# Optimization experiments

Hardware: AMD Instinct MI355X
Metric: run time of the kernel (lower is better)

The kernel has to match this reference:

```python
import jax, jax.numpy as jnp
import numpy as np

B, H, E = 32768, 1024, 512
VOCAB = 1600 * 20  # input_dim * 20


def setup_inputs() -> dict:
    key = jax.random.key(0)
    ks = jax.random.split(key, 13)
    sc_e = 1.0 / np.sqrt(E)
    sc_h = 1.0 / np.sqrt(H)
    sc_2h = 1.0 / np.sqrt(2 * H)
    # weights stored as [in, out] (transpose of torch Linear.weight)
    return {
        "s_t_minus_1": jax.random.normal(ks[0], (B, 1, H), jnp.float32),
        "y_t_minus_1": jax.random.randint(ks[1], (B, 1), 0, VOCAB, jnp.int64 if jax.config.jax_enable_x64 else jnp.int32),
        "c_t": jax.random.normal(ks[2], (B, 1, 2 * H), jnp.float32),
        "emb": jax.random.normal(ks[3], (VOCAB, E), jnp.float32),
        "Wz": jax.random.uniform(ks[4], (E, H), jnp.float32, -sc_e, sc_e),
        "Uz": jax.random.uniform(ks[5], (H, H), jnp.float32, -sc_h, sc_h),
        "Cz": jax.random.uniform(ks[6], (2 * H, H), jnp.float32, -sc_2h, sc_2h),
        "Wr": jax.random.uniform(ks[7], (E, H), jnp.float32, -sc_e, sc_e),
        "Ur": jax.random.uniform(ks[8], (H, H), jnp.float32, -sc_h, sc_h),
        "Cr": jax.random.uniform(ks[9], (2 * H, H), jnp.float32, -sc_2h, sc_2h),
        "W": jax.random.uniform(ks[10], (E, H), jnp.float32, -sc_e, sc_e),
        "U": jax.random.uniform(ks[11], (H, H), jnp.float32, -sc_h, sc_h),
        "C": jax.random.uniform(ks[12], (2 * H, H), jnp.float32, -sc_2h, sc_2h),
    }


def reference(s_t_minus_1, y_t_minus_1, c_t, emb, Wz, Uz, Cz, Wr, Ur, Cr, W, U, C):
    # embedding lookup: (B,1) -> (B,1,E)
    y = emb[y_t_minus_1]
    # gates, all contractions over last axis
    z_t = jax.nn.sigmoid(y @ Wz + s_t_minus_1 @ Uz + c_t @ Cz)  # (B,1,H)
    r_t = jax.nn.sigmoid(y @ Wr + s_t_minus_1 @ Ur + c_t @ Cr)  # (B,1,H)
    s_tilde = jnp.tanh(y @ W + (r_t * s_t_minus_1) @ U + c_t @ C)
    s_t = (1.0 - z_t) * s_t_minus_1 + z_t * s_tilde
    return s_t
```

## Files before the change

### kernel.cpp

```cpp
#include <hip/hip_runtime.h>

typedef unsigned short u16;
typedef float  f32x4   __attribute__((ext_vector_type(4)));
typedef float  f32x16  __attribute__((ext_vector_type(16)));
typedef short  bf16x8  __attribute__((ext_vector_type(8)));
typedef u16    u16x8   __attribute__((ext_vector_type(8)));

#define BROWS 32768
#define KTOT  3584
#define NKT   (KTOT / 64)

static __device__ __forceinline__ u16 f2b(float f) {
    unsigned x = __float_as_uint(f);
    x += 0x7fffu + ((x >> 16) & 1u);
    return (u16)(x >> 16);
}
static __device__ __forceinline__ float b2f(u16 u) {
    return __uint_as_float(((unsigned)u) << 16);
}
static __device__ __forceinline__ float sigm(float x) {
    return 1.f / (1.f + __expf(-x));
}
static __device__ __forceinline__ float tanh_s(float x) {
    float ax = fabsf(x);
    float e  = __expf(-2.f * ax);
    float t  = (1.f - e) / (1.f + e);
    return copysignf(t, x);
}
static __device__ __forceinline__ void gld16(const u16* g, u16* l) {
    __builtin_amdgcn_global_load_lds(
        (const __attribute__((address_space(1))) void*)g,
        (__attribute__((address_space(3))) void*)l, 16, 0, 0);
}

__global__ __launch_bounds__(256) void pack_x(
    const float* __restrict__ s, const int* __restrict__ y,
    const float* __restrict__ c, const float* __restrict__ emb,
    u16* __restrict__ X)
{
    long tid = (long)blockIdx.x * 256 + threadIdx.x;
    int  row = (int)(tid / 448);
    int  seg = (int)(tid % 448);
    int  e0  = seg * 8;
    const float* src;
    if (e0 < 512)        src = emb + (long)y[row] * 512 + e0;
    else if (e0 < 1536)  src = s   + (long)row * 1024 + (e0 - 512);
    else                 src = c   + (long)row * 2048 + (e0 - 1536);
    f32x4 a = *(const f32x4*)src;
    f32x4 b = *(const f32x4*)(src + 4);
    u16x8 o;
    o[0]=f2b(a[0]); o[1]=f2b(a[1]); o[2]=f2b(a[2]); o[3]=f2b(a[3]);
    o[4]=f2b(b[0]); o[5]=f2b(b[1]); o[6]=f2b(b[2]); o[7]=f2b(b[3]);
    *(u16x8*)&X[(long)row * KTOT + e0] = o;
}

__global__ __launch_bounds__(256) void wtrans_all(
    const float* __restrict__ Wz, const float* __restrict__ Uz,
    const float* __restrict__ Cz, const float* __restrict__ Wr,
    const float* __restrict__ Ur, const float* __restrict__ Cr,
    const float* __restrict__ W,  const float* __restrict__ U,
    const float* __restrict__ C,
    u16* __restrict__ WzrT, u16* __restrict__ W2T)
{
    __shared__ float t[32][33];
    int z = blockIdx.z;
    const float* src; u16* dst; int kd;
    switch (z) {
        case 0: src = Wz; dst = WzrT + 0;                  kd = 512;  break;
        case 1: src = Uz; dst = WzrT + 512;                kd = 1024; break;
        case 2: src = Cz; dst = WzrT + 1536;               kd = 2048; break;
        case 3: src = Wr; dst = WzrT + 1024 * KTOT;        kd = 512;  break;
        case 4: src = Ur; dst = WzrT + 1024 * KTOT + 512;  kd = 1024; break;
        case 5: src = Cr; dst = WzrT + 1024 * KTOT + 1536; kd = 2048; break;
        case 6: src = W;  dst = W2T + 0;                   kd = 512;  break;
        case 7: src = U;  dst = W2T + 512;                 kd = 1024; break;
        default: src = C; dst = W2T + 1536;                kd = 2048; break;
    }
    int k0 = blockIdx.x * 32;
    if (k0 >= kd) return;
    int n0 = blockIdx.y * 32;
    int tx = threadIdx.x, ty = threadIdx.y;
    #pragma unroll
    for (int r = ty; r < 32; r += 8)
        t[r][tx] = src[(long)(k0 + r) * 1024 + n0 + tx];
    __syncthreads();
    #pragma unroll
    for (int r = ty; r < 32; r += 8)
        dst[(long)(n0 + r) * KTOT + k0 + tx] = f2b(t[tx][r]);
}


#define RDA32(P,mt,ks) a[mt][ks] = *(const bf16x8*)((P) + (mt)*2048 + ((ks)>>1)*512 + (((ks)&1) ? laneX : laneO))
#define RDB32(P,nt,ks) b[nt][ks] = *(const bf16x8*)((P) + (nt)*2048 + ((ks)>>1)*512 + (((ks)&1) ? laneX : laneO))
#define RDA_T(P,mt) RDA32(P,mt,0); RDA32(P,mt,1); RDA32(P,mt,2); RDA32(P,mt,3)
#define RDB_T(P,nt) RDB32(P,nt,0); RDB32(P,nt,1); RDB32(P,nt,2); RDB32(P,nt,3)
#define MM32(mt,nt,ks) acc[mt][nt] = __builtin_amdgcn_mfma_f32_32x32x16_bf16(a[mt][ks], b[nt][ks], acc[mt][nt], 0, 0, 0)
#define MMQ32(m0,m1,nt) \
    MM32(m0,nt,0); MM32(m1,nt,0); MM32(m0,nt,1); MM32(m1,nt,1); \
    MM32(m0,nt,2); MM32(m1,nt,2); MM32(m0,nt,3); MM32(m1,nt,3)

#define PH_MID \
    __builtin_amdgcn_s_barrier(); \
    asm volatile("s_waitcnt lgkmcnt(0)" ::: "memory"); \
    __builtin_amdgcn_sched_barrier(0); \
    __builtin_amdgcn_s_setprio(1);

#define PH_END \
    __builtin_amdgcn_s_setprio(0); \
    __builtin_amdgcn_sched_barrier(0); \
    __builtin_amdgcn_s_barrier();

template<int MODE>
__global__ __launch_bounds__(512, 1) void gemm8(
    const u16* __restrict__ Xc, const u16* __restrict__ rsin,
    const u16* __restrict__ Wt,
    u16* __restrict__ zb, u16* __restrict__ rsb,
    const u16* __restrict__ zread, float* __restrict__ out, int NT)
{
    extern __shared__ u16 smem[];

    int bid = blockIdx.x, nwg = gridDim.x;
    int q   = nwg >> 3;
    int wg  = (bid & 7) * q + (bid >> 3);
    int bm  = wg / NT, bn = wg % NT;
    int R0  = bm * 256;
    int C0  = bn * 256;

    int t = threadIdx.x, w = t >> 6, l = t & 63;
    int wr = w >> 2, wc = w & 3;

    int rl   = l >> 2;
    int ccl  = ((l & 3) * 8) ^ ((l >> 5) * 16) ^ (((w >> 1) & 1) * 8);
    int sr0  = w >> 1, sc = w & 1;
    int colb = sc * 32 + ccl;
    int offAx[2][2], offAr[2][2], offB[2][2];
    #pragma unroll
    for (int h = 0; h < 2; h++)
        #pragma unroll
        for (int i = 0; i < 2; i++) {
            int row = h * 128 + (sr0 + i * 4) * 16 + rl;
            offAx[h][i] = (R0 + row) * KTOT + colb;
            offAr[h][i] = (R0 + row) * 1024 + colb - 512;
            offB [h][i] = (C0 + row) * KTOT + colb;
        }

    auto stageA = [&](int kt) {
        int k0 = kt * 64;
        u16* Ld = smem + (kt & 1) * 32768;
        bool useR = (MODE == 1) && (k0 >= 512) && (k0 < 1536);
        #pragma unroll
        for (int h = 0; h < 2; h++)
            #pragma unroll
            for (int i = 0; i < 2; i++) {
                const u16* g = useR ? (rsin + (offAr[h][i] + k0))
                                    : (Xc   + (offAx[h][i] + k0));
                gld16(g, Ld + h * 8192 + (w + i * 8) * 512);
            }
    };
    auto stageB = [&](int kt) {
        int k0 = kt * 64;
        u16* Ld = smem + (kt & 1) * 32768 + 16384;
        #pragma unroll
        for (int h = 0; h < 2; h++)
            #pragma unroll
            for (int i = 0; i < 2; i++)
                gld16(Wt + (offB[h][i] + k0),
                      Ld + h * 8192 + (w + i * 8) * 512);
    };

    int laneO = ((l >> 4) & 1) * 1024 + (l & 15) * 32
              + ((((l >> 5) * 8) ^ (((l >> 3) & 1) * 16)) ^ (((l >> 4) & 1) * 8));
    int laneX = laneO ^ 16;

    f32x16 acc[4][2];
    #pragma unroll
    for (int mt = 0; mt < 4; mt++)
        #pragma unroll
        for (int nt = 0; nt < 2; nt++)
            acc[mt][nt] = (f32x16)(0.f);

    bf16x8 a[4][4], b[2][4];

    int aoff = wr * 8192;
    int boff = 16384 + wc * 4096;
    const u16* Ae = smem + aoff;
    const u16* Be = smem + boff;
    const u16* Ao = Ae + 32768;
    const u16* Bo = Be + 32768;

    stageA(0); stageB(0);
    stageA(1); stageB(1);
    asm volatile("s_waitcnt vmcnt(8)" ::: "memory");
    __builtin_amdgcn_s_barrier();
    RDA_T(Ae, 0); RDA_T(Ae, 1); RDB_T(Be, 0);

    for (int kt = 0; kt < NKT; ++kt) {
        int bs = kt & 1;
        const u16* Ab = smem + bs * 32768 + aoff;
        const u16* Bb = smem + bs * 32768 + boff;
        const u16* An = smem + (bs ^ 1) * 32768 + aoff;
        const u16* Bn = smem + (bs ^ 1) * 32768 + boff;

        PH_MID; MMQ32(0, 1, 0); RDB_T(Bb, 1); PH_END;
        PH_MID; MMQ32(0, 1, 1); RDA_T(Ab, 2); RDA_T(Ab, 3); PH_END;
        if (kt + 2 < NKT) stageB(kt + 2);
        PH_MID; MMQ32(2, 3, 1); PH_END;
        if (kt + 2 < NKT) {
            stageA(kt + 2);
            asm volatile("s_waitcnt vmcnt(8)" ::: "memory");
        } else {
            asm volatile("s_waitcnt vmcnt(0)" ::: "memory");
        }
        PH_MID; MMQ32(2, 3, 0);
        if (kt + 1 < NKT) { RDA_T(An, 0); RDA_T(An, 1); RDB_T(Bn, 0); }
        PH_END;
    }

    int hi4 = (l >> 5) * 4, lc32 = l & 31;
    long R0w = R0 + wr * 128;
    int  C0w = C0 + wc * 64;
    if (MODE == 0) {
        if (C0 < 1024) {
            #pragma unroll
            for (int mt = 0; mt < 4; mt++)
                #pragma unroll
                for (int nt = 0; nt < 2; nt++) {
                    int col = C0w + nt * 32 + lc32;
                    #pragma unroll
                    for (int qq = 0; qq < 4; qq++)
                        #pragma unroll
                        for (int jj = 0; jj < 4; jj++) {
                            long r = R0w + mt * 32 + qq * 8 + hi4 + jj;
                            zb[r * 1024 + col] = f2b(sigm(acc[mt][nt][qq * 4 + jj]));
                        }
                }
        } else {
            #pragma unroll
            for (int mt = 0; mt < 4; mt++)
                #pragma unroll
                for (int nt = 0; nt < 2; nt++) {
                    int h = C0w + nt * 32 + lc32 - 1024;
                    #pragma unroll
                    for (int qq = 0; qq < 4; qq++)
                        #pragma unroll
                        for (int jj = 0; jj < 4; jj++) {
                            long r = R0w + mt * 32 + qq * 8 + hi4 + jj;
                            float sv = b2f(Xc[r * KTOT + 512 + h]);
                            float rr = sigm(acc[mt][nt][qq * 4 + jj]);
                            rsb[r * 1024 + h] = f2b(rr * sv);
                        }
                }
        }
    } else {
        #pragma unroll
        for (int mt = 0; mt < 4; mt++)
            #pragma unroll
            for (int nt = 0; nt < 2; nt++) {
                int col = C0w + nt * 32 + lc32;
                #pragma unroll
                for (int qq = 0; qq < 4; qq++)
                    #pragma unroll
                    for (int jj = 0; jj < 4; jj++) {
                        long r = R0w + mt * 32 + qq * 8 + hi4 + jj;
                        float st = tanh_s(acc[mt][nt][qq * 4 + jj]);
                        float z  = b2f(zread[r * 1024 + col]);
                        float sv = b2f(Xc[r * KTOT + 512 + col]);
                        out[r * 1024 + col] = fmaf(z, st - sv, sv);
                    }
            }
    }
}

extern "C" void kernel_launch(void* const* d_in, const int* in_sizes, int n_in,
                              void* d_out, int out_size, void* d_ws, size_t ws_size,
                              hipStream_t stream)
{
    const float* s   = (const float*)d_in[0];
    const int*   y   = (const int*)  d_in[1];
    const float* c   = (const float*)d_in[2];
    const float* emb = (const float*)d_in[3];
    const float* Wz  = (const float*)d_in[4];
    const float* Uz  = (const float*)d_in[5];
    const float* Cz  = (const float*)d_in[6];
    const float* Wr  = (const float*)d_in[7];
    const float* Ur  = (const float*)d_in[8];
    const float* Cr  = (const float*)d_in[9];
    const float* W   = (const float*)d_in[10];
    const float* U   = (const float*)d_in[11];
    const float* C   = (const float*)d_in[12];
    float* out = (float*)d_out;

    char* ws = (char*)d_ws;
    u16* Xcat = (u16*)(ws);
    u16* rsb  = (u16*)(ws + 234881024);
    u16* zbuf = (u16*)(ws + 301989888);
    u16* WzrT = (u16*)(ws + 369098752);
    u16* W2T  = (u16*)(ws + 383778816);

    hipFuncSetAttribute((const void*)gemm8<0>,
                        hipFuncAttributeMaxDynamicSharedMemorySize, 131072);
    hipFuncSetAttribute((const void*)gemm8<1>,
                        hipFuncAttributeMaxDynamicSharedMemorySize, 131072);

    pack_x<<<BROWS * 448 / 256, 256, 0, stream>>>(s, y, c, emb, Xcat);

    dim3 tb(32, 8);
    wtrans_all<<<dim3(64, 32, 9), tb, 0, stream>>>(
        Wz, Uz, Cz, Wr, Ur, Cr, W, U, C, WzrT, W2T);

    gemm8<0><<<(BROWS / 256) * (2048 / 256), 512, 131072, stream>>>(
        Xcat, nullptr, WzrT, zbuf, rsb, nullptr, nullptr, 2048 / 256);

    gemm8<1><<<(BROWS / 256) * (1024 / 256), 512, 131072, stream>>>(
        Xcat, rsb, W2T, nullptr, nullptr, zbuf, out, 1024 / 256);
}
```

Measured before the change: 835.1 us.

## Switch GEMM main loop to 32-wide K tiles with 4-stage LDS ring buffer

Result: slower. 858.3 us (+2.8%).

```diff
diff --git a/kernel.cpp b/kernel.cpp
--- a/kernel.cpp
+++ b/kernel.cpp
@@ -8,7 +8,7 @@
 
 #define BROWS 32768
 #define KTOT  3584
-#define NKT   (KTOT / 64)
+#define NKT   (KTOT / 32)
 
 static __device__ __forceinline__ u16 f2b(float f) {
     unsigned x = __float_as_uint(f);
@@ -90,14 +90,12 @@
 }
 
 
-#define RDA32(P,mt,ks) a[mt][ks] = *(const bf16x8*)((P) + (mt)*2048 + ((ks)>>1)*512 + (((ks)&1) ? laneX : laneO))
-#define RDB32(P,nt,ks) b[nt][ks] = *(const bf16x8*)((P) + (nt)*2048 + ((ks)>>1)*512 + (((ks)&1) ? laneX : laneO))
-#define RDA_T(P,mt) RDA32(P,mt,0); RDA32(P,mt,1); RDA32(P,mt,2); RDA32(P,mt,3)
-#define RDB_T(P,nt) RDB32(P,nt,0); RDB32(P,nt,1); RDB32(P,nt,2); RDB32(P,nt,3)
+#define RDA32(P,mt,ks) a[mt][ks] = *(const bf16x8*)((P) + (mt)*1024 + ((ks) ? laneX : laneO))
+#define RDB32(P,nt,ks) b[nt][ks] = *(const bf16x8*)((P) + (nt)*1024 + ((ks) ? laneX : laneO))
 #define MM32(mt,nt,ks) acc[mt][nt] = __builtin_amdgcn_mfma_f32_32x32x16_bf16(a[mt][ks], b[nt][ks], acc[mt][nt], 0, 0, 0)
-#define MMQ32(m0,m1,nt) \
-    MM32(m0,nt,0); MM32(m1,nt,0); MM32(m0,nt,1); MM32(m1,nt,1); \
-    MM32(m0,nt,2); MM32(m1,nt,2); MM32(m0,nt,3); MM32(m1,nt,3)
+#define MMMT2(m0,m1) \
+    MM32(m0,0,0); MM32(m1,0,0); MM32(m0,1,0); MM32(m1,1,0); \
+    MM32(m0,0,1); MM32(m1,0,1); MM32(m0,1,1); MM32(m1,1,1)
 
 #define PH_MID \
     __builtin_amdgcn_s_barrier(); \
@@ -129,46 +127,37 @@
     int t = threadIdx.x, w = t >> 6, l = t & 63;
     int wr = w >> 2, wc = w & 3;
 
-    int rl   = l >> 2;
-    int ccl  = ((l & 3) * 8) ^ ((l >> 5) * 16) ^ (((w >> 1) & 1) * 8);
-    int sr0  = w >> 1, sc = w & 1;
-    int colb = sc * 32 + ccl;
-    int offAx[2][2], offAr[2][2], offB[2][2];
+    int rl  = l >> 2;
+    int ccl = ((l & 3) * 8) ^ ((l >> 5) * 16) ^ ((w & 1) * 8);
+    int offAx[2], offAr[2], offB2[2];
     #pragma unroll
-    for (int h = 0; h < 2; h++)
+    for (int i = 0; i < 2; i++) {
+        int row = (w + i * 8) * 16 + rl;
+        offAx[i] = (R0 + row) * KTOT + ccl;
+        offAr[i] = (R0 + row) * 1024 + ccl - 512;
+        offB2[i] = (C0 + row) * KTOT + ccl;
+    }
+
+    auto stA = [&](int kt, int ob) {
+        int k0 = kt * 32;
+        u16* Ld = smem + ob;
+        bool useR = (MODE == 1) && (k0 >= 512) && (k0 < 1536);
         #pragma unroll
         for (int i = 0; i < 2; i++) {
-            int row = h * 128 + (sr0 + i * 4) * 16 + rl;
-            offAx[h][i] = (R0 + row) * KTOT + colb;
-            offAr[h][i] = (R0 + row) * 1024 + colb - 512;
-            offB [h][i] = (C0 + row) * KTOT + colb;
-        }
-
-    auto stageA = [&](int kt) {
-        int k0 = kt * 64;
-        u16* Ld = smem + (kt & 1) * 32768;
-        bool useR = (MODE == 1) && (k0 >= 512) && (k0 < 1536);
+            const u16* g = useR ? (rsin + offAr[i] + k0)
+                                : (Xc   + offAx[i] + k0);
+            gld16(g, Ld + (w + i * 8) * 512);
+        }
+    };
+    auto stB = [&](int kt, int ob) {
+        int k0 = kt * 32;
+        u16* Ld = smem + ob + 8192;
         #pragma unroll
-        for (int h = 0; h < 2; h++)
-            #pragma unroll
-            for (int i = 0; i < 2; i++) {
-                const u16* g = useR ? (rsin + (offAr[h][i] + k0))
-                                    : (Xc   + (offAx[h][i] + k0));
-                gld16(g, Ld + h * 8192 + (w + i * 8) * 512);
-            }
+        for (int i = 0; i < 2; i++)
+            gld16(Wt + offB2[i] + k0, Ld + (w + i * 8) * 512);
     };
-    auto stageB = [&](int kt) {
-        int k0 = kt * 64;
-        u16* Ld = smem + (kt & 1) * 32768 + 16384;
-        #pragma unroll
-        for (int h = 0; h < 2; h++)
-            #pragma unroll
-            for (int i = 0; i < 2; i++)
-                gld16(Wt + (offB[h][i] + k0),
-                      Ld + h * 8192 + (w + i * 8) * 512);
-    };
-
-    int laneO = ((l >> 4) & 1) * 1024 + (l & 15) * 32
+
+    int laneO = ((l >> 4) & 1) * 512 + (l & 15) * 32
               + ((((l >> 5) * 8) ^ (((l >> 3) & 1) * 16)) ^ (((l >> 4) & 1) * 8));
     int laneX = laneO ^ 16;
 
@@ -179,41 +168,54 @@
         for (int nt = 0; nt < 2; nt++)
             acc[mt][nt] = (f32x16)(0.f);
 
-    bf16x8 a[4][4], b[2][4];
-
-    int aoff = wr * 8192;
-    int boff = 16384 + wc * 4096;
-    const u16* Ae = smem + aoff;
-    const u16* Be = smem + boff;
-    const u16* Ao = Ae + 32768;
-    const u16* Bo = Be + 32768;
-
-    stageA(0); stageB(0);
-    stageA(1); stageB(1);
+    bf16x8 a[4][2], b[2][2];
+
+    int abase = wr * 4096;
+    int bbase = 8192 + wc * 2048;
+
+    int oc = 0, on = 16384, o2 = 32768, os = 49152;
+    stB(0, oc); stA(0, oc);
+    stB(1, on); stA(1, on);
+    stB(2, o2); stA(2, o2);
     asm volatile("s_waitcnt vmcnt(8)" ::: "memory");
     __builtin_amdgcn_s_barrier();
-    RDA_T(Ae, 0); RDA_T(Ae, 1); RDB_T(Be, 0);
+    {
+        const u16* Ac = smem + oc + abase;
+        const u16* Bc = smem + oc + bbase;
+        RDA32(Ac,0,0); RDA32(Ac,0,1); RDA32(Ac,1,0); RDA32(Ac,1,1);
+        RDA32(Ac,2,0); RDA32(Ac,2,1); RDA32(Ac,3,0); RDA32(Ac,3,1);
+        RDB32(Bc,0,0); RDB32(Bc,0,1); RDB32(Bc,1,0); RDB32(Bc,1,1);
+    }
 
     for (int kt = 0; kt < NKT; ++kt) {
-        int bs = kt & 1;
-        const u16* Ab = smem + bs * 32768 + aoff;
-        const u16* Bb = smem + bs * 32768 + boff;
-        const u16* An = smem + (bs ^ 1) * 32768 + aoff;
-        const u16* Bn = smem + (bs ^ 1) * 32768 + boff;
-
-        PH_MID; MMQ32(0, 1, 0); RDB_T(Bb, 1); PH_END;
-        PH_MID; MMQ32(0, 1, 1); RDA_T(Ab, 2); RDA_T(Ab, 3); PH_END;
-        if (kt + 2 < NKT) stageB(kt + 2);
-        PH_MID; MMQ32(2, 3, 1); PH_END;
-        if (kt + 2 < NKT) {
-            stageA(kt + 2);
-            asm volatile("s_waitcnt vmcnt(8)" ::: "memory");
+        const u16* An = smem + on + abase;
+        const u16* Bn = smem + on + bbase;
+
+        if (kt <= NKT - 4) {
+            stB(kt + 3, os);
+            asm volatile("s_waitcnt vmcnt(6)" ::: "memory");
+        } else if (kt == NKT - 3) {
+            asm volatile("s_waitcnt vmcnt(4)" ::: "memory");
         } else {
             asm volatile("s_waitcnt vmcnt(0)" ::: "memory");
         }
-        PH_MID; MMQ32(2, 3, 0);
-        if (kt + 1 < NKT) { RDA_T(An, 0); RDA_T(An, 1); RDB_T(Bn, 0); }
+        PH_MID;
+        MMMT2(0, 1);
+        if (kt + 1 < NKT) {
+            RDA32(An,0,0); RDA32(An,0,1); RDA32(An,1,0); RDA32(An,1,1);
+        }
         PH_END;
+
+        if (kt <= NKT - 4) stA(kt + 3, os);
+        PH_MID;
+        MMMT2(2, 3);
+        if (kt + 1 < NKT) {
+            RDA32(An,2,0); RDA32(An,2,1); RDA32(An,3,0); RDA32(An,3,1);
+            RDB32(Bn,0,0); RDB32(Bn,0,1); RDB32(Bn,1,0); RDB32(Bn,1,1);
+        }
+        PH_END;
+
+        int tmp = oc; oc = on; on = o2; o2 = os; os = tmp;
     }
 
     int hi4 = (l >> 5) * 4, lc32 = l & 31;
```
